# Performance work log

Hardware: AMD Instinct MI355X
Metric: run time of the kernel (lower is better)

Reference implementation:

```python
import jax, jax.numpy as jnp
import numpy as np

# ---- static config (matches init_kwargs) ----
B, SX, SY, SZ = 1, 64, 64, 64
W = 32            # HIDDEN_DIM
L = 4             # num_fourier_layers
M1 = M2 = M3 = 8  # fourier modes per axis
PX = PY = PZ = 8  # domain padding
ALPHA = 0.05      # leaky relu slope
OUTC = 6


def conv3d(x, w, pad):
    # x: (B,C,D,H,W), w: (O,I,kd,kh,kw)
    return jax.lax.conv_general_dilated(
        x, w, window_strides=(1, 1, 1), padding=[(pad, pad)] * 3,
        dimension_numbers=('NCDHW', 'OIDHW', 'NCDHW'))


def pad1(x):
    # periodic=(0,0,0) -> zero pad 1 on every spatial side (matches ZeroPad3d chain)
    return jnp.pad(x, ((0, 0), (0, 0), (1, 1), (1, 1), (1, 1)))


def basic_block(x, w1, w2):
    # BasicBlock3D_Periodic with use_shortcut=False
    out = jax.nn.leaky_relu(conv3d(pad1(x), w1, 0), ALPHA)
    return conv3d(pad1(out), w2, 0)


def spec_apply(xft_slice, w):
    # xft_slice: complex (B,C,d1,d2,d3); w: (2C,2C,5,5,5)
    re_im = jnp.concatenate([xft_slice.real, xft_slice.imag], axis=1)  # (B,2C,...)
    out = conv3d(re_im, w, 2)                                          # (B,2C,...)
    b, c2, d1, d2, d3 = out.shape
    out = out.reshape(b, c2 // 2, 2, d1, d2, d3)
    return jax.lax.complex(out[:, :, 0], out[:, :, 1])


def spectral_conv(x, ws):
    # ws: (8, 2W, 2W, 5, 5, 5); mode-limited per-octant conv in frequency space
    b, c, n, m, l = x.shape
    xft = jnp.fft.rfftn(x, axes=(-3, -2, -1))  # (b,c,n,m,l//2+1) complex
    out = jnp.zeros((b, c, n, m, l // 2 + 1), dtype=xft.dtype)
    octs = [
        (slice(None, M1),  slice(None, M2)),
        (slice(n - M1, None), slice(None, M2)),
        (slice(None, M1),  slice(m - M2, None)),
        (slice(n - M1, None), slice(m - M2, None)),
        (slice(M1, n - M1), slice(None, M2)),
        (slice(None, M1),  slice(M2, m - M2)),
        (slice(M1, n - M1), slice(m - M2, None)),
        (slice(n - M1, None), slice(M2, m - M2)),
    ]
    for i, (s1, s2) in enumerate(octs):
        out = out.at[:, :, s1, s2, :M3].set(spec_apply(xft[:, :, s1, s2, :M3], ws[i]))
    return jnp.fft.irfftn(out, s=(n, m, l), axes=(-3, -2, -1))


def setup_inputs() -> dict:
    key = jax.random.key(0)
    ks = jax.random.split(key, 16)
    f32 = jnp.float32
    d = {
        'yeex': jax.random.normal(ks[0], (B, SX, SY, SZ), f32),
        'yeey': jax.random.normal(ks[1], (B, SX, SY, SZ), f32),
        'yeez': jax.random.normal(ks[2], (B, SX, SY, SZ), f32),
        'fc0_w': jax.random.normal(ks[3], (6, W), f32) * 0.1,
        'fc0_b': jax.random.normal(ks[4], (W,), f32) * 0.01,
        'spec_w': jax.random.normal(ks[5], (L, 8, 2 * W, 2 * W, 5, 5, 5), f32) * 0.02,
        'blk_w1': jax.random.normal(ks[6], (L, W, W, 3, 3, 3), f32) * 0.05,
        'blk_w2': jax.random.normal(ks[7], (L, W, W, 3, 3, 3), f32) * 0.05,
        'fc1_w': jax.random.normal(ks[8], (W, 128), f32) * 0.05,
        'fc1_b': jax.random.normal(ks[9], (128,), f32) * 0.01,
        'fc2_w': jax.random.normal(ks[10], (128, OUTC), f32) * 0.05,
        'fc2_b': jax.random.normal(ks[11], (OUTC,), f32) * 0.01,
    }
    return d


def reference(yeex, yeey, yeez, fc0_w, fc0_b, spec_w, blk_w1, blk_w2,
              fc1_w, fc1_b, fc2_w, fc2_b):
    b, sx, sy, sz = yeez.shape
    # normalized coordinate grid (3 channels), as in standard FNO get_grid
    gx = jnp.broadcast_to(jnp.linspace(0., 1., sx, dtype=yeex.dtype)[None, :, None, None], (b, sx, sy, sz))
    gy = jnp.broadcast_to(jnp.linspace(0., 1., sy, dtype=yeex.dtype)[None, None, :, None], (b, sx, sy, sz))
    gz = jnp.broadcast_to(jnp.linspace(0., 1., sz, dtype=yeex.dtype)[None, None, None, :], (b, sx, sy, sz))
    inp = jnp.stack([yeex, yeey, yeez, gx, gy, gz], axis=-1)  # (b,sx,sy,sz,6)

    x = inp @ fc0_w + fc0_b                      # lift: (b,sx,sy,sz,W)
    x = jnp.transpose(x, (0, 4, 1, 2, 3))        # (b,W,sx,sy,sz)
    x = jnp.pad(x, ((0, 0), (0, 0), (0, PX), (0, PY), (0, PZ)))

    for i in range(L):
        x1 = spectral_conv(x, spec_w[i])
        x2 = basic_block(x, blk_w1[i], blk_w2[i])
        x = x1 + x2 + x
        if i < L - 1:
            x = jax.nn.leaky_relu(x, ALPHA)

    x = x[:, :, :sx, :sy, :sz]                   # crop domain padding
    x = jnp.transpose(x, (0, 2, 3, 4, 1))        # (b,sx,sy,sz,W)
    x = jax.nn.leaky_relu(x @ fc1_w + fc1_b, ALPHA)
    return x @ fc2_w + fc2_b                     # (b,sx,sy,sz,OUTC)
```

## Files before the change

kernel.cpp:

```cpp
#include <hip/hip_runtime.h>
#include <math.h>

#define NS 72
#define NS2 (NS*NS)
#define NS3 (NS*NS*NS)
#define MZ 8
#define LALPHA 0.05f
#define CSCALE (1.0f/256.0f)

typedef _Float16 f16x8 __attribute__((ext_vector_type(8)));
typedef _Float16 f16x4 __attribute__((ext_vector_type(4)));
typedef float f32x4 __attribute__((ext_vector_type(4)));

__device__ __forceinline__ float leakyf(float v){ return v > 0.f ? v : LALPHA*v; }

__constant__ int c_RX0[8] = {0,64,0,64, 8,0,8,64};
__constant__ int c_RNX[8] = {8,8,8,8, 56,8,56,8};
__constant__ int c_RY0[8] = {0,0,64,64, 0,8,64,8};
__constant__ int c_RNY[8] = {8,8,8,8, 8,56,8,56};
__constant__ int c_Bbase[8] = {0,1728,3456,5184, 6912,15552,24192,32832};
__constant__ int c_BY[8]    = {12,12,12,12, 12,60,12,60};

__global__ void k_tw(float2* tw){
  int t = threadIdx.x;
  if (t < NS){
    double th = (2.0*M_PI/72.0)*(double)t;
    tw[t] = make_float2((float)cos(th), (float)sin(th));
  }
}

__global__ void k_fc0(const float* __restrict__ yx, const float* __restrict__ yy,
                      const float* __restrict__ yz, const float* __restrict__ w,
                      const float* __restrict__ b, float* __restrict__ X){
  int idx = blockIdx.x*256 + threadIdx.x;
  int z = idx % NS; int t = idx / NS; int y = t % NS; t /= NS; int x = t % NS; int c = t / NS;
  float v = 0.f;
  if (x < 64 && y < 64 && z < 64){
    int p = (x*64 + y)*64 + z;
    float i0 = yx[p], i1 = yy[p], i2 = yz[p];
    float gx = (float)x*(1.f/63.f), gy = (float)y*(1.f/63.f), gz = (float)z*(1.f/63.f);
    v = b[c] + i0*w[0*32+c] + i1*w[1*32+c] + i2*w[2*32+c]
             + gx*w[3*32+c] + gy*w[4*32+c] + gz*w[5*32+c];
  }
  X[idx] = v;
}

__global__ void k_zdft(const float* __restrict__ X, float2* __restrict__ A, const float2* __restrict__ tw){
  __shared__ float2 stw[NS];
  int tid = threadIdx.x;
  if (tid < NS) stw[tid] = tw[tid];
  __syncthreads();
  int f = blockIdx.x*256 + tid;
  const float* row = X + (size_t)f*NS;
  float ar[MZ], ai[MZ]; int tk[MZ];
  #pragma unroll
  for (int k=0;k<MZ;k++){ ar[k]=0.f; ai[k]=0.f; tk[k]=0; }
  for (int z=0; z<NS; z++){
    float v = row[z];
    #pragma unroll
    for (int k=0;k<MZ;k++){
      float2 w = stw[tk[k]];
      ar[k] += v*w.x;
      ai[k] -= v*w.y;
      tk[k] += k; if (tk[k] >= NS) tk[k] -= NS;
    }
  }
  float2* o = A + (size_t)f*MZ;
  #pragma unroll
  for (int k=0;k<MZ;k++) o[k] = make_float2(ar[k], ai[k]);
}

__global__ void k_ydft(const float2* __restrict__ A, float2* __restrict__ B, const float2* __restrict__ tw){
  __shared__ float2 stw[NS];
  int tid = threadIdx.x;
  if (tid < NS) stw[tid] = tw[tid];
  __syncthreads();
  int f = blockIdx.x*256 + tid;
  int ky = f % NS; int cx = f / NS;
  const float2* in = A + (size_t)cx*NS*MZ;
  float ar[MZ], ai[MZ];
  #pragma unroll
  for (int k=0;k<MZ;k++){ ar[k]=0.f; ai[k]=0.f; }
  int t = 0;
  for (int y=0;y<NS;y++){
    float2 w = stw[t]; t += ky; if (t>=NS) t-=NS;
    const float2* iy = in + y*MZ;
    #pragma unroll
    for (int k=0;k<MZ;k++){
      float2 v = iy[k];
      ar[k] += v.x*w.x + v.y*w.y;
      ai[k] += v.y*w.x - v.x*w.y;
    }
  }
  float2* o = B + (size_t)f*MZ;
  #pragma unroll
  for (int k=0;k<MZ;k++) o[k] = make_float2(ar[k], ai[k]);
}

__global__ void k_xdftL(const float2* __restrict__ B, float2* __restrict__ C, const float2* __restrict__ tw){
  __shared__ float2 stw[NS];
  int tid = threadIdx.x;
  if (tid < NS) stw[tid] = tw[tid];
  __syncthreads();
  int t = blockIdx.x*256 + tid;
  int h = t & 1; int t2 = t >> 1;
  int c = t2 >> 11; int l = t2 & 2047;
  int kx, ky;
  if (l < 576){ ky = l & 7; kx = l >> 3; }
  else if (l < 1152){ int e = l - 576; ky = 64 + (e & 7); kx = e >> 3; }
  else { int e = l - 1152; int kyi = e >> 4; int kxi = e & 15;
         ky = 8 + kyi; kx = (kxi < 8) ? kxi : 56 + kxi; }
  int k0 = h*4;
  const float2* in = B + ((size_t)c*NS2 + ky)*MZ + k0;
  float ar[4], ai[4];
  #pragma unroll
  for (int k=0;k<4;k++){ ar[k]=0.f; ai[k]=0.f; }
  int tt = 0;
  for (int x=0;x<NS;x++){
    float2 w = stw[tt]; tt += kx; if (tt>=NS) tt-=NS;
    const float2* ix = in + (size_t)x*NS*MZ;
    #pragma unroll
    for (int k=0;k<4;k++){
      float2 v = ix[k];
      ar[k] += v.x*w.x + v.y*w.y;
      ai[k] += v.y*w.x - v.x*w.y;
    }
  }
  float2* o = C + (((size_t)c*NS + kx)*NS + ky)*MZ + k0;
  #pragma unroll
  for (int k=0;k<4;k++) o[k] = make_float2(ar[k], ai[k]);
}

__global__ void k_wpackh(const float* __restrict__ W, _Float16* __restrict__ Ah){
  int e = blockIdx.x*256 + threadIdx.x;
  int i = e & 63; int o = (e>>6) & 63;
  int t2 = e >> 12; int tap = t2 % 125; int r = t2 / 125;
  const float* wr = W + (size_t)r*64*64*125;
  Ah[e] = (_Float16)wr[((size_t)(o*64 + (i&1)*32 + (i>>1)))*125 + tap];
}

__global__ void k_cpackh(const float2* __restrict__ C, _Float16* __restrict__ Bg){
  int g = blockIdx.x*256 + threadIdx.x;
  int ci = g & 31; int elem = g >> 5;
  int r = 0;
  #pragma unroll
  for (int k=1;k<8;k++) if (elem >= c_Bbase[k]) r = k;
  int el = elem - c_Bbase[r];
  int BY = c_BY[r];
  int q3 = el % 12; int tt = el / 12; int q2 = tt % BY; int q1 = tt / BY;
  int kxr = q1-2, kyr = q2-2, kzr = q3-2;
  float2 v = make_float2(0.f,0.f);
  if ((unsigned)kxr < (unsigned)c_RNX[r] && (unsigned)kyr < (unsigned)c_RNY[r] && (unsigned)kzr < 8u){
    v = C[(((size_t)ci*NS + (c_RX0[r]+kxr))*NS + (c_RY0[r]+kyr))*MZ + kzr];
  }
  _Float16* o = Bg + (size_t)elem*64 + 2*ci;
  o[0] = (_Float16)(v.x*CSCALE);
  o[1] = (_Float16)(v.y*CSCALE);
}

__global__ __launch_bounds__(64) void k_freqmfma(const _Float16* __restrict__ Ah,
                                                 const _Float16* __restrict__ Bg,
                                                 float* __restrict__ Pp){
  int gb = blockIdx.x;
  int ks = gb >> 8; int b = gb & 255;
  int r, til;
  if (b < 32){ r = b>>3; til = b&7; }
  else       { r = 4 + (b-32)/56; til = (b-32)%56; }
  int BY = c_BY[r];
  int q1, q2base;
  if (r==5 || r==7){ q1 = 2 + til/7; q2base = 2 + (til%7)*8; }
  else             { q1 = 2 + til;   q2base = 2; }
  int lane = threadIdx.x;
  int l15 = lane & 15, kg = lane >> 4;
  int q2l = q2base + (l15>>3), q3l = 2 + (l15&7);
  const _Float16* Ar = Ah + (size_t)r*125*4096;
  const _Float16* Br = Bg + (size_t)c_Bbase[r]*64;
  int lb = q2l*12 + q3l;
  f32x4 acc[4][4];
  f32x4 zz = {0.f,0.f,0.f,0.f};
  #pragma unroll
  for (int m=0;m<4;m++)
    #pragma unroll
    for (int n=0;n<4;n++) acc[m][n] = zz;
  int t0 = ks*16;
  int t1 = t0+16 < 125 ? t0+16 : 125;
  for (int tt=t0; tt<t1; tt++){
    int td = tt/25; int rm = tt - td*25; int th = rm/5; int tz = rm - th*5;
    const _Float16* At = Ar + tt*4096;
    f16x8 a[4][2];
    #pragma unroll
    for (int mt=0;mt<4;mt++){
      a[mt][0] = *(const f16x8*)(At + (mt*16+l15)*64 + kg*8);
      a[mt][1] = *(const f16x8*)(At + (mt*16+l15)*64 + 32 + kg*8);
    }
    int ebase = (q1 + td - 2)*BY*12 + lb + (th-2)*12 + (tz-2);
    f16x8 bf[4][2];
    #pragma unroll
    for (int nt=0;nt<4;nt++){
      const _Float16* bp = Br + (size_t)(ebase + nt*24)*64 + kg*8;
      bf[nt][0] = *(const f16x8*)(bp);
      bf[nt][1] = *(const f16x8*)(bp + 32);
    }
    #pragma unroll
    for (int mt=0;mt<4;mt++)
      #pragma unroll
      for (int nt=0;nt<4;nt++){
        acc[mt][nt] = __builtin_amdgcn_mfma_f32_16x16x32_f16(a[mt][0], bf[nt][0], acc[mt][nt],0,0,0);
        acc[mt][nt] = __builtin_amdgcn_mfma_f32_16x16x32_f16(a[mt][1], bf[nt][1], acc[mt][nt],0,0,0);
      }
  }
  float* base = Pp + (((size_t)ks*256 + b)*64 + lane)*64;
  #pragma unroll
  for (int mt=0;mt<4;mt++)
    #pragma unroll
    for (int nt=0;nt<4;nt++)
      *(f32x4*)(base + mt*16 + nt*4) = acc[mt][nt];
}

__global__ void k_fred(const float* __restrict__ Pp, float* __restrict__ Df){
  int t = blockIdx.x*256 + threadIdx.x;
  int mtnt = t & 15; int lane = (t>>4) & 63; int b = t >> 10;
  int mt = mtnt >> 2, nt = mtnt & 3;
  int r, til;
  if (b < 32){ r = b>>3; til = b&7; }
  else       { r = 4 + (b-32)/56; til = (b-32)%56; }
  int x0 = c_RX0[r], y0 = c_RY0[r];
  int q1, q2base;
  if (r==5 || r==7){ q1 = 2 + til/7; q2base = 2 + (til%7)*8; }
  else             { q1 = 2 + til;   q2base = 2; }
  int l15 = lane & 15, kg = lane >> 4;
  int q2l = q2base + (l15>>3), q3l = 2 + (l15&7);
  f32x4 s = {0.f,0.f,0.f,0.f};
  #pragma unroll
  for (int ks=0;ks<8;ks++){
    s += *(const f32x4*)(Pp + (((size_t)ks*256 + b)*64 + lane)*64 + mtnt*4);
  }
  int kx = x0 + q1 - 2;
  int kz = q3l - 2;
  int ky = y0 + q2l + nt*2 - 2;
  #pragma unroll
  for (int rg=0;rg<4;rg++){
    int o = mt*16 + kg*4 + rg;
    int co = o >> 1, reim = o & 1;
    Df[((((size_t)co*NS + kx)*NS + ky)*MZ + kz)*2 + reim] = s[rg]*256.0f;
  }
}

__global__ void k_invx(const float2* __restrict__ D, float2* __restrict__ E, const float2* __restrict__ tw){
  __shared__ float2 stw[NS];
  int tid = threadIdx.x;
  if (tid < NS) stw[tid] = tw[tid];
  __syncthreads();
  int f = blockIdx.x*256 + tid;
  int ky = f % NS; int t2 = f / NS; int x = t2 % NS; int c = t2 / NS;
  const float2* in = D + ((size_t)c*NS2 + ky)*MZ;
  float ar[MZ], ai[MZ];
  #pragma unroll
  for (int k=0;k<MZ;k++){ ar[k]=0.f; ai[k]=0.f; }
  int t = 0;
  for (int kx=0;kx<NS;kx++){
    float2 w = stw[t]; t += x; if (t>=NS) t-=NS;
    const float2* ix = in + (size_t)kx*NS*MZ;
    #pragma unroll
    for (int k=0;k<MZ;k++){
      float2 v = ix[k];
      ar[k] += v.x*w.x - v.y*w.y;
      ai[k] += v.x*w.y + v.y*w.x;
    }
  }
  float2* o = E + (size_t)f*MZ;
  #pragma unroll
  for (int k=0;k<MZ;k++) o[k] = make_float2(ar[k]*(1.f/72.f), ai[k]*(1.f/72.f));
}

__global__ void k_invyz(const float2* __restrict__ E, _Float16* __restrict__ X1h, const float2* __restrict__ tw){
  __shared__ float2 stw[NS];
  int tid = threadIdx.x;
  if (tid < NS) stw[tid] = tw[tid];
  __syncthreads();
  int f = blockIdx.x*256 + tid;
  int y = f % NS; int t2 = f / NS; int x = t2 % NS; int c = t2 / NS;
  const float2* in = E + ((size_t)c*NS + x)*NS*MZ;
  float ar[MZ], ai[MZ];
  #pragma unroll
  for (int k=0;k<MZ;k++){ ar[k]=0.f; ai[k]=0.f; }
  int t = 0;
  for (int ky=0;ky<NS;ky++){
    float2 w = stw[t]; t += y; if (t>=NS) t-=NS;
    const float2* ik = in + ky*MZ;
    #pragma unroll
    for (int k=0;k<MZ;k++){
      float2 v = ik[k];
      ar[k] += v.x*w.x - v.y*w.y;
      ai[k] += v.x*w.y + v.y*w.x;
    }
  }
  const float scale = 1.f/(72.f*72.f);
  _Float16* o = X1h + (size_t)f*NS;
  int tk[MZ];
  #pragma unroll
  for (int k=0;k<MZ;k++) tk[k]=0;
  for (int z=0; z<NS; z++){
    float acc = ar[0];
    #pragma unroll
    for (int k=1;k<MZ;k++){
      float2 w = stw[tk[k]];
      acc += 2.f*(ar[k]*w.x - ai[k]*w.y);
      tk[k] += k; if (tk[k] >= NS) tk[k] -= NS;
    }
    o[z] = (_Float16)(acc*scale);
  }
}


__global__ void k_wcvt2(const float* __restrict__ w1, const float* __restrict__ w2,
                        _Float16* __restrict__ WhA, _Float16* __restrict__ WhB){
  int e = blockIdx.x*256 + threadIdx.x;
  int h = e >= 27648; int e2 = e - (h ? 27648 : 0);
  int tap = e2 >> 10; int co = (e2>>5)&31; int ci = e2&31;
  const float* w = h ? w2 : w1;
  _Float16* o = h ? WhB : WhA;
  o[e2] = (_Float16)w[(co*32+ci)*27 + tap];
}

__global__ void k_cvt16(const float* __restrict__ Xf, _Float16* __restrict__ Xg){
  int b = blockIdx.x;
  int tid = threadIdx.x;
  if (b >= 1458){
    _Float16* g = (b==1458) ? (Xg - 4096) : (Xg + (size_t)NS3*32);
    f16x8 zz = {0,0,0,0,0,0,0,0};
    f16x8* gp = (f16x8*)g;
    gp[tid] = zz; gp[tid+256] = zz;
    return;
  }
  int p = b*256 + tid;
  f16x8 o0,o1,o2,o3;
  #pragma unroll
  for (int c=0;c<8;c++){
    o0[c] = (_Float16)Xf[(size_t)c*NS3 + p];
    o1[c] = (_Float16)Xf[(size_t)(c+8)*NS3 + p];
    o2[c] = (_Float16)Xf[(size_t)(c+16)*NS3 + p];
    o3[c] = (_Float16)Xf[(size_t)(c+24)*NS3 + p];
  }
  f16x8* op = (f16x8*)(Xg + (size_t)p*32);
  op[0]=o0; op[1]=o1; op[2]=o2; op[3]=o3;
}

__global__ void k_zgH(_Float16* __restrict__ Hg){
  int e = blockIdx.x*256 + threadIdx.x;
  _Float16* g = (e < 512) ? (Hg - 4096 + e*8)
                          : (Hg + (size_t)NS3*32 + (size_t)(e-512)*8);
  f16x8 zz = {0,0,0,0,0,0,0,0};
  *(f16x8*)g = zz;
}

__global__ __launch_bounds__(256) void k_convm(const _Float16* __restrict__ Xg,
    const _Float16* __restrict__ Wh, float* __restrict__ OUT, _Float16* __restrict__ OUTH,
    const _Float16* __restrict__ X1h, const _Float16* __restrict__ XresH,
    int mode2, int do_leaky){
  int tid = threadIdx.x;
  int orig = blockIdx.x;
  int xcd = orig & 7, loc = orig >> 3;
  int wg = (xcd < 2 ? xcd*183 : 366 + (xcd-2)*182) + loc;
  int j = wg*4 + (tid>>6);
  int slab = j/81, nb = j - slab*81;
  int q0 = nb*64;
  int lane = tid & 63;
  int l15 = lane & 15, kg = lane >> 4;
  f32x4 acc[2][4];
  f32x4 zz = {0.f,0.f,0.f,0.f};
  #pragma unroll
  for (int a=0;a<2;a++)
    #pragma unroll
    for (int b=0;b<4;b++) acc[a][b] = zz;
  int wbase = l15*32 + kg*8;
  int bofs  = l15*32 + kg*8;
  for (int dx=0; dx<3; dx++){
    int xx = slab + dx - 1;
    if ((unsigned)xx >= 72u) continue;
    const _Float16* Xrow = Xg + ((size_t)xx*5184 + q0)*32;
    const _Float16* Wdx  = Wh + dx*9216;
    f16x8 pa0[2], pa1[2], pb0[2], pb1[2], pb2[2], pb3[2];
    {
      const _Float16* wp = Wdx + wbase;
      pa0[0] = *(const f16x8*)(wp);
      pa1[0] = *(const f16x8*)(wp + 512);
      const _Float16* bb = Xrow + (-73)*32 + bofs;
      pb0[0] = *(const f16x8*)(bb);
      pb1[0] = *(const f16x8*)(bb + 512);
      pb2[0] = *(const f16x8*)(bb + 1024);
      pb3[0] = *(const f16x8*)(bb + 1536);
    }
    #pragma unroll
    for (int t9=0; t9<9; t9++){
      int cur = t9 & 1, nxt = cur ^ 1;
      if (t9 < 8){
        int tn = t9 + 1;
        int off = ((tn/3)-1)*72 + (tn%3) - 1;
        const _Float16* wp = Wdx + tn*1024 + wbase;
        pa0[nxt] = *(const f16x8*)(wp);
        pa1[nxt] = *(const f16x8*)(wp + 512);
        const _Float16* bb = Xrow + off*32 + bofs;
        pb0[nxt] = *(const f16x8*)(bb);
        pb1[nxt] = *(const f16x8*)(bb + 512);
        pb2[nxt] = *(const f16x8*)(bb + 1024);
        pb3[nxt] = *(const f16x8*)(bb + 1536);
      }
      acc[0][0] = __builtin_amdgcn_mfma_f32_16x16x32_f16(pa0[cur],pb0[cur],acc[0][0],0,0,0);
      acc[0][1] = __builtin_amdgcn_mfma_f32_16x16x32_f16(pa0[cur],pb1[cur],acc[0][1],0,0,0);
      acc[0][2] = __builtin_amdgcn_mfma_f32_16x16x32_f16(pa0[cur],pb2[cur],acc[0][2],0,0,0);
      acc[0][3] = __builtin_amdgcn_mfma_f32_16x16x32_f16(pa0[cur],pb3[cur],acc[0][3],0,0,0);
      acc[1][0] = __builtin_amdgcn_mfma_f32_16x16x32_f16(pa1[cur],pb0[cur],acc[1][0],0,0,0);
      acc[1][1] = __builtin_amdgcn_mfma_f32_16x16x32_f16(pa1[cur],pb1[cur],acc[1][1],0,0,0);
      acc[1][2] = __builtin_amdgcn_mfma_f32_16x16x32_f16(pa1[cur],pb2[cur],acc[1][2],0,0,0);
      acc[1][3] = __builtin_amdgcn_mfma_f32_16x16x32_f16(pa1[cur],pb3[cur],acc[1][3],0,0,0);
    }
  }
  if (mode2){
    #pragma unroll
    for (int nt=0; nt<4; nt++){
      int q = q0 + nt*16 + l15;
      int y = q/72, z = q - y*72;
      bool edge = (y==0)||(y==71)||(z==0)||(z==71);
      #pragma unroll
      for (int c2=0;c2<2;c2++){
        #pragma unroll
        for (int r=0;r<4;r++){
          int co = c2*16 + kg*4 + r;
          size_t idx = (size_t)co*NS3 + (size_t)slab*5184 + q;
          float v = acc[c2][nt][r];
          if (!edge){
            v += (float)X1h[idx] + (float)XresH[((size_t)slab*5184 + q)*32 + co];
            if (do_leaky) v = leakyf(v);
          }
          OUT[idx] = v;
        }
      }
    }
  } else {
    #pragma unroll
    for (int nt=0; nt<4; nt++){
      int q = q0 + nt*16 + l15;
      int y = q/72, z = q - y*72;
      bool edge = (y==0)||(y==71)||(z==0)||(z==71);
      _Float16* hp = OUTH + ((size_t)slab*5184 + q)*32 + kg*4;
      #pragma unroll
      for (int c2=0;c2<2;c2++){
        f32x4 av = acc[c2][nt];
        f16x4 hv;
        #pragma unroll
        for (int r=0;r<4;r++){
          float v = av[r];
          if (!edge) v = leakyf(v);
          hv[r] = (_Float16)v;
        }
        *(f16x4*)(hp + c2*16) = hv;
      }
    }
  }
}

__global__ void k_corrH(_Float16* __restrict__ H, const _Float16* __restrict__ Xg,
                        const _Float16* __restrict__ Wh){
  int t = blockIdx.x*256 + threadIdx.x;
  int co = t & 31; int t2 = t >> 5;
  int e = t2 % 284; int x = t2 / 284;
  int y, z;
  if (e < 72){ y = 0; z = e; }
  else if (e < 144){ y = 71; z = e - 72; }
  else if (e < 214){ z = 0; y = e - 143; }
  else { z = 71; y = e - 213; }
  int q = y*72 + z;
  float corr = 0.f;
  for (int tap=0; tap<27; tap++){
    int dx = tap/9, rr = tap%9, dy = rr/3, dz = rr%3;
    int xx = x + dx - 1;
    if ((unsigned)xx >= 72u) continue;
    int yy = y + dy - 1, zz = z + dz - 1;
    if ((unsigned)yy < 72u && (unsigned)zz < 72u) continue;
    int lin = (xx*5184 + q + (dy-1)*72 + (dz-1))*32;
    const _Float16* V = Xg + lin;
    const _Float16* Wr = Wh + (tap*32 + co)*32;
    float s = 0.f;
    #pragma unroll
    for (int ci=0; ci<32; ci++) s += (float)V[ci]*(float)Wr[ci];
    corr += s;
  }
  size_t idx = ((size_t)x*5184 + q)*32 + co;
  float v = (float)H[idx] - corr;
  v = leakyf(v);
  H[idx] = (_Float16)v;
}

__global__ void k_corr(float* __restrict__ OUT, const _Float16* __restrict__ Xg,
                       const _Float16* __restrict__ Wh, const _Float16* __restrict__ X1h,
                       const _Float16* __restrict__ XresH, int mode2, int do_leaky){
  int t = blockIdx.x*256 + threadIdx.x;
  int co = t & 31; int t2 = t >> 5;
  int e = t2 % 284; int x = t2 / 284;
  int y, z;
  if (e < 72){ y = 0; z = e; }
  else if (e < 144){ y = 71; z = e - 72; }
  else if (e < 214){ z = 0; y = e - 143; }
  else { z = 71; y = e - 213; }
  int q = y*72 + z;
  float corr = 0.f;
  for (int tap=0; tap<27; tap++){
    int dx = tap/9, rr = tap%9, dy = rr/3, dz = rr%3;
    int xx = x + dx - 1;
    if ((unsigned)xx >= 72u) continue;
    int yy = y + dy - 1, zz = z + dz - 1;
    if ((unsigned)yy < 72u && (unsigned)zz < 72u) continue;
    int lin = (xx*5184 + q + (dy-1)*72 + (dz-1))*32;
    const _Float16* V = Xg + lin;
    const _Float16* Wr = Wh + (tap*32 + co)*32;
    float s = 0.f;
    #pragma unroll
    for (int ci=0; ci<32; ci++) s += (float)V[ci]*(float)Wr[ci];
    corr += s;
  }
  size_t idx = (size_t)co*NS3 + (size_t)x*5184 + q;
  float v = OUT[idx] - corr;
  if (mode2) v += (float)X1h[idx] + (float)XresH[((size_t)x*5184 + q)*32 + co];
  if (do_leaky) v = leakyf(v);
  OUT[idx] = v;
}

__global__ void k_head(const float* __restrict__ X, const float* __restrict__ w1, const float* __restrict__ b1,
                       const float* __restrict__ w2, const float* __restrict__ b2, float* __restrict__ out){
  __shared__ float s1t[32*128];
  __shared__ float sb1[128];
  __shared__ float s2[128*6];
  __shared__ float sb2[6];
  int tid = threadIdx.x;
  for (int e=tid;e<4096;e+=256){ int j=e>>5, c=e&31; s1t[e]=w1[c*128+j]; }
  if (tid<128) sb1[tid]=b1[tid];
  for (int e=tid;e<768;e+=256) s2[e]=w2[e];
  if (tid<6) sb2[tid]=b2[tid];
  __syncthreads();
  int p0 = blockIdx.x*256 + tid;
  float xin[2][32];
  float acc[2][6];
  #pragma unroll
  for (int vv=0; vv<2; vv++){
    int p = p0 + vv*131072;
    int z = p % 64; int t = p / 64; int y = t % 64; int x = t / 64;
    size_t q = ((size_t)x*NS + y)*NS + z;
    #pragma unroll
    for (int c=0;c<32;c++) xin[vv][c] = X[(size_t)c*NS3 + q];
    #pragma unroll
    for (int o=0;o<6;o++) acc[vv][o]=sb2[o];
  }
  for (int j=0;j<128;j++){
    const float4* wj = (const float4*)(s1t + j*32);
    float h0 = sb1[j], h1 = h0;
    #pragma unroll
    for (int c4=0;c4<8;c4++){
      float4 w = wj[c4];
      h0 += xin[0][c4*4+0]*w.x + xin[0][c4*4+1]*w.y + xin[0][c4*4+2]*w.z + xin[0][c4*4+3]*w.w;
      h1 += xin[1][c4*4+0]*w.x + xin[1][c4*4+1]*w.y + xin[1][c4*4+2]*w.z + xin[1][c4*4+3]*w.w;
    }
    h0 = leakyf(h0); h1 = leakyf(h1);
    const float* s2j = s2 + j*6;
    #pragma unroll
    for (int o=0;o<6;o++){
      float wv = s2j[o];
      acc[0][o] += h0*wv;
      acc[1][o] += h1*wv;
    }
  }
  #pragma unroll
  for (int vv=0; vv<2; vv++){
    float* O = out + (size_t)(p0 + vv*131072)*6;
    #pragma unroll
    for (int o=0;o<6;o++) O[o]=acc[vv][o];
  }
}

extern "C" void kernel_launch(void* const* d_in, const int* in_sizes, int n_in,
                              void* d_out, int out_size, void* d_ws, size_t ws_size,
                              hipStream_t stream) {
  const float* yeex = (const float*)d_in[0];
  const float* yeey = (const float*)d_in[1];
  const float* yeez = (const float*)d_in[2];
  const float* fc0w = (const float*)d_in[3];
  const float* fc0b = (const float*)d_in[4];
  const float* specw= (const float*)d_in[5];
  const float* bw1  = (const float*)d_in[6];
  const float* bw2  = (const float*)d_in[7];
  const float* fc1w = (const float*)d_in[8];
  const float* fc1b = (const float*)d_in[9];
  const float* fc2w = (const float*)d_in[10];
  const float* fc2b = (const float*)d_in[11];
  float* out = (float*)d_out;
  float* ws  = (float*)d_ws;

  float*  P0 = ws;
  float*  X1s = ws + 11943936;
  float*  P2 = ws + 23887872;
  float2* A  = (float2*)(ws + 35831808);
  float2* B  = (float2*)(ws + 41140224);
  float2* Cf = (float2*)(ws + 46448640);
  float2* Df = (float2*)(ws + 51757056);
  float2* TW = (float2*)(ws + 57065472);
  _Float16* Ah = (_Float16*)A;
  _Float16* Bg = (_Float16*)B;
  float*    Pp = X1s;
  _Float16* X1h = (_Float16*)X1s;
  _Float16* XhG = (_Float16*)(ws + 35831808) + 4096;
  _Float16* HhG = (_Float16*)(ws + 41807872) + 4096;
  _Float16* WhA = (_Float16*)(ws + 47783936);
  _Float16* WhB = (_Float16*)(ws + 47797760);

  float* curX = P0; float* curY = P2;

  k_tw<<<1,128,0,stream>>>(TW);
  k_fc0<<<46656,256,0,stream>>>(yeex,yeey,yeez,fc0w,fc0b,curX);
  for (int i=0;i<4;i++){
    k_zdft<<<648,256,0,stream>>>(curX, A, TW);
    k_ydft<<<648,256,0,stream>>>(A, B, TW);
    k_xdftL<<<512,256,0,stream>>>(B, Cf, TW);
    k_wpackh<<<16000,256,0,stream>>>(specw + (size_t)i*8*64*64*125, Ah);
    k_cpackh<<<5184,256,0,stream>>>(Cf, Bg);
    hipMemsetAsync(Df, 0, (size_t)1327104*8, stream);
    k_freqmfma<<<2048,64,0,stream>>>(Ah, Bg, Pp);
    k_fred<<<1024,256,0,stream>>>(Pp, (float*)Df);
    k_invx<<<648,256,0,stream>>>(Df, A, TW);
    k_invyz<<<648,256,0,stream>>>(A, X1h, TW);
    k_wcvt2<<<216,256,0,stream>>>(bw1 + (size_t)i*27648, bw2 + (size_t)i*27648, WhA, WhB);
    k_cvt16<<<1460,256,0,stream>>>(curX, XhG);
    k_zgH<<<4,256,0,stream>>>(HhG);
    k_convm<<<1458,256,0,stream>>>(XhG, WhA, nullptr, HhG, nullptr, nullptr, 0, 1);
    k_corrH<<<2556,256,0,stream>>>(HhG, XhG, WhA);
    k_convm<<<1458,256,0,stream>>>(HhG, WhB, curY, nullptr, X1h, XhG, 1, (i<3)?1:0);
    k_corr<<<2556,256,0,stream>>>(curY, HhG, WhB, X1h, XhG, 1, (i<3)?1:0);
    float* tmp = curX; curX = curY; curY = tmp;
  }
  k_head<<<512,256,0,stream>>>(curX, fc1w, fc1b, fc2w, fc2b, out);
}
```

Baseline: 2.413 ms.

## Skip zero kx modes in inverse x-DFT, vectorize DFT loads/stores, tune convm occupancy

In the inverse x-transform, rows with ky between 8 and 63 have non-zero spectral data only at kx<8 and kx>=64, so the loop skips the known-zero band. The thread index mapping is reordered so ky varies slowest, which keeps warps uniform on the branch and changes the access pattern while the output is still written in the original layout. The forward z-DFT now reads input rows with float4 loads and the inverse yz kernel writes fp16 results four at a time. The main conv kernel gets a min-blocks launch bound of 2, which may cap its registers and risk spills.

```diff
diff --git a/kernel.cpp b/kernel.cpp
--- a/kernel.cpp
+++ b/kernel.cpp
@@ -55,14 +55,19 @@
   float ar[MZ], ai[MZ]; int tk[MZ];
   #pragma unroll
   for (int k=0;k<MZ;k++){ ar[k]=0.f; ai[k]=0.f; tk[k]=0; }
-  for (int z=0; z<NS; z++){
-    float v = row[z];
-    #pragma unroll
-    for (int k=0;k<MZ;k++){
-      float2 w = stw[tk[k]];
-      ar[k] += v*w.x;
-      ai[k] -= v*w.y;
-      tk[k] += k; if (tk[k] >= NS) tk[k] -= NS;
+  for (int z4=0; z4<NS; z4+=4){
+    float4 v4 = *(const float4*)(row + z4);
+    float vs[4] = {v4.x, v4.y, v4.z, v4.w};
+    #pragma unroll
+    for (int zz=0; zz<4; zz++){
+      float v = vs[zz];
+      #pragma unroll
+      for (int k=0;k<MZ;k++){
+        float2 w = stw[tk[k]];
+        ar[k] += v*w.x;
+        ai[k] -= v*w.y;
+        tk[k] += k; if (tk[k] >= NS) tk[k] -= NS;
+      }
     }
   }
   float2* o = A + (size_t)f*MZ;
@@ -252,23 +257,49 @@
   if (tid < NS) stw[tid] = tw[tid];
   __syncthreads();
   int f = blockIdx.x*256 + tid;
-  int ky = f % NS; int t2 = f / NS; int x = t2 % NS; int c = t2 / NS;
+  int ky = f / 2304; int rem = f - ky*2304;
+  int c = rem / NS; int x = rem - c*NS;
   const float2* in = D + ((size_t)c*NS2 + ky)*MZ;
   float ar[MZ], ai[MZ];
   #pragma unroll
   for (int k=0;k<MZ;k++){ ar[k]=0.f; ai[k]=0.f; }
-  int t = 0;
-  for (int kx=0;kx<NS;kx++){
-    float2 w = stw[t]; t += x; if (t>=NS) t-=NS;
-    const float2* ix = in + (size_t)kx*NS*MZ;
-    #pragma unroll
-    for (int k=0;k<MZ;k++){
-      float2 v = ix[k];
-      ar[k] += v.x*w.x - v.y*w.y;
-      ai[k] += v.x*w.y + v.y*w.x;
-    }
-  }
-  float2* o = E + (size_t)f*MZ;
+  if (ky >= 8 && ky < 64){
+    int t = 0;
+    for (int kx=0;kx<8;kx++){
+      float2 w = stw[t]; t += x; if (t>=NS) t-=NS;
+      const float2* ix = in + (size_t)kx*NS*MZ;
+      #pragma unroll
+      for (int k=0;k<MZ;k++){
+        float2 v = ix[k];
+        ar[k] += v.x*w.x - v.y*w.y;
+        ai[k] += v.x*w.y + v.y*w.x;
+      }
+    }
+    t = (64*x) % NS;
+    for (int kx=64;kx<NS;kx++){
+      float2 w = stw[t]; t += x; if (t>=NS) t-=NS;
+      const float2* ix = in + (size_t)kx*NS*MZ;
+      #pragma unroll
+      for (int k=0;k<MZ;k++){
+        float2 v = ix[k];
+        ar[k] += v.x*w.x - v.y*w.y;
+        ai[k] += v.x*w.y + v.y*w.x;
+      }
+    }
+  } else {
+    int t = 0;
+    for (int kx=0;kx<NS;kx++){
+      float2 w = stw[t]; t += x; if (t>=NS) t-=NS;
+      const float2* ix = in + (size_t)kx*NS*MZ;
+      #pragma unroll
+      for (int k=0;k<MZ;k++){
+        float2 v = ix[k];
+        ar[k] += v.x*w.x - v.y*w.y;
+        ai[k] += v.x*w.y + v.y*w.x;
+      }
+    }
+  }
+  float2* o = E + (((size_t)c*NS + x)*NS + ky)*MZ;
   #pragma unroll
   for (int k=0;k<MZ;k++) o[k] = make_float2(ar[k]*(1.f/72.f), ai[k]*(1.f/72.f));
 }
@@ -300,15 +331,20 @@
   int tk[MZ];
   #pragma unroll
   for (int k=0;k<MZ;k++) tk[k]=0;
-  for (int z=0; z<NS; z++){
-    float acc = ar[0];
-    #pragma unroll
-    for (int k=1;k<MZ;k++){
-      float2 w = stw[tk[k]];
-      acc += 2.f*(ar[k]*w.x - ai[k]*w.y);
-      tk[k] += k; if (tk[k] >= NS) tk[k] -= NS;
-    }
-    o[z] = (_Float16)(acc*scale);
+  for (int z4=0; z4<NS; z4+=4){
+    f16x4 hv;
+    #pragma unroll
+    for (int zz=0; zz<4; zz++){
+      float acc = ar[0];
+      #pragma unroll
+      for (int k=1;k<MZ;k++){
+        float2 w = stw[tk[k]];
+        acc += 2.f*(ar[k]*w.x - ai[k]*w.y);
+        tk[k] += k; if (tk[k] >= NS) tk[k] -= NS;
+      }
+      hv[zz] = (_Float16)(acc*scale);
+    }
+    *(f16x4*)(o + z4) = hv;
   }
 }
 
@@ -354,7 +390,7 @@
   *(f16x8*)g = zz;
 }
 
-__global__ __launch_bounds__(256) void k_convm(const _Float16* __restrict__ Xg,
+__global__ __launch_bounds__(256,2) void k_convm(const _Float16* __restrict__ Xg,
     const _Float16* __restrict__ Wh, float* __restrict__ OUT, _Float16* __restrict__ OUTH,
     const _Float16* __restrict__ X1h, const _Float16* __restrict__ XresH,
     int mode2, int do_leaky){
```

Measured after the change: 2.381 ms. No clear change (-1.4%).
